# Kernel optimization log

Measured on AMD Instinct MI355X. Metric: run time of the kernel, lower is better.

Reference implementation:

```python
import jax, jax.numpy as jnp
import numpy as np

T, B, D = 1024, 512, 128
NQ = 8          # n_qubits == hidden_dim
H = NQ


def setup_inputs() -> dict:
    key = jax.random.key(0)
    ks = jax.random.split(key, 13)
    fan_in = D + H
    s = 1.0 / np.sqrt(fan_in)
    def lin(kw, kb):
        W = jax.random.uniform(kw, (NQ, fan_in), jnp.float32, -s, s)
        b = jax.random.uniform(kb, (NQ,), jnp.float32, -s, s)
        return W, b
    Wf, bf = lin(ks[0], ks[1])
    Wi, bi = lin(ks[2], ks[3])
    Wu, bu = lin(ks[4], ks[5])
    Wo, bo = lin(ks[6], ks[7])
    qwf = jax.random.normal(ks[8], (NQ,), jnp.float32)
    qwi = jax.random.normal(ks[9], (NQ,), jnp.float32)
    qwu = jax.random.normal(ks[10], (NQ,), jnp.float32)
    qwo = jax.random.normal(ks[11], (NQ,), jnp.float32)
    inputs = jax.random.normal(ks[12], (T, B, D), jnp.float32)
    return {"inputs": inputs,
            "Wf": Wf, "bf": bf, "Wi": Wi, "bi": bi,
            "Wu": Wu, "bu": bu, "Wo": Wo, "bo": bo,
            "qwf": qwf, "qwi": qwi, "qwu": qwu, "qwo": qwo}


def _qgate(z, qw):
    # Analytic form of the circuit: RX(x_i) then RY(w_i) per wire, CNOT ladder,
    # expval(Z_0). Z_0 commutes with the CNOT ladder, so only wire 0 matters:
    # <Z_0> = cos(x_0) * cos(w_0). Gate = sigmoid(<Z_0>), shape [B].
    return jax.nn.sigmoid(jnp.cos(z[:, 0]) * jnp.cos(qw[0]))


def reference(inputs, Wf, bf, Wi, bi, Wu, bu, Wo, bo, qwf, qwi, qwu, qwo):
    batch = inputs.shape[1]
    hx0 = jnp.zeros((batch, H), inputs.dtype)
    cx0 = jnp.zeros((batch, H), inputs.dtype)

    def step(carry, x):
        hx, cx = carry
        comb = jnp.concatenate([x, hx], axis=1)          # [B, D+H]
        f = _qgate(comb @ Wf.T + bf, qwf)                # [B]
        i = _qgate(comb @ Wi.T + bi, qwi)                # [B]
        g = jnp.tanh(comb @ Wu.T + bu)                   # [B, H]
        o = _qgate(comb @ Wo.T + bo, qwo)                # [B]
        cx = f[:, None] * cx + i[:, None] * g
        hx = o[:, None] * jnp.tanh(cx)
        return (hx, cx), hx

    (hx, cx), outputs = jax.lax.scan(step, (hx0, cx0), inputs)
    return outputs, hx, cx
```

## Files before the change

### kernel.cpp

```cpp
#include <hip/hip_runtime.h>
#include <cstddef>

#define TT 1024
#define BB 512
#define DD 128
#define FAN 136

__device__ __forceinline__ float v_exp2(float x){ float d; asm("v_exp_f32 %0, %1" : "=v"(d) : "v"(x)); return d; }
__device__ __forceinline__ float v_rcp (float x){ float d; asm("v_rcp_f32 %0, %1" : "=v"(d) : "v"(x)); return d; }
__device__ __forceinline__ float v_cosr(float x){ float d; asm("v_cos_f32 %0, %1" : "=v"(d) : "v"(x)); return d; }

__device__ __forceinline__ float fast_cos(float x){
    float r = x * 0.15915494309189535f;
    r = r - floorf(r);
    return v_cosr(r);
}
__device__ __forceinline__ float fast_sigmoid(float x){
    float e = v_exp2(x * -1.4426950408889634f);
    return v_rcp(1.0f + e);
}
__device__ __forceinline__ float fast_tanh(float x){
    float e = v_exp2(x * 2.8853900817779268f);
    return 1.0f - 2.0f * v_rcp(e + 1.0f);
}

__global__ __launch_bounds__(256) void qlstm_zx(
    const float* __restrict__ x,
    const float* __restrict__ Wf, const float* __restrict__ bf,
    const float* __restrict__ Wi, const float* __restrict__ bi,
    const float* __restrict__ Wu, const float* __restrict__ bu,
    const float* __restrict__ Wo, const float* __restrict__ bo,
    float* __restrict__ Z)
{
    __shared__ float xs[256 * 33];
    const int tid = threadIdx.x;
    const int t  = blockIdx.x >> 1;
    const int b0 = (blockIdx.x & 1) * 256;

    float acc[8];
    #pragma unroll
    for (int k = 0; k < 8; ++k) acc[k] = bu[k];
    float af = bf[0], ai = bi[0], ao = bo[0];

    const float* xbase = x + ((size_t)t * BB + b0) * DD;

    for (int dc = 0; dc < 4; ++dc) {
        #pragma unroll
        for (int i = 0; i < 8; ++i) {
            int idx = i * 256 + tid;
            int row = idx >> 3, cg = idx & 7;
            const float4 v = *reinterpret_cast<const float4*>(xbase + row * DD + dc * 32 + cg * 4);
            float* d = &xs[row * 33 + cg * 4];
            d[0] = v.x; d[1] = v.y; d[2] = v.z; d[3] = v.w;
        }
        __syncthreads();

        const int base = dc * 32;
        #pragma unroll
        for (int d = 0; d < 32; ++d) {
            const float xv = xs[tid * 33 + d];
            const int wc = base + d;
            #pragma unroll
            for (int k = 0; k < 8; ++k) acc[k] = fmaf(xv, Wu[k * FAN + wc], acc[k]);
            af = fmaf(xv, Wf[wc], af);
            ai = fmaf(xv, Wi[wc], ai);
            ao = fmaf(xv, Wo[wc], ao);
        }
        __syncthreads();
    }

    float* zb = Z + (size_t)t * 12 * BB + b0 + tid;
    #pragma unroll
    for (int k = 0; k < 8; ++k) zb[k * BB] = acc[k];
    zb[8 * BB] = af; zb[9 * BB] = ai; zb[10 * BB] = ao;
}

__global__ __launch_bounds__(64) void qlstm_rec(
    const float* __restrict__ Z,
    const float* __restrict__ Wf, const float* __restrict__ Wi,
    const float* __restrict__ Wu, const float* __restrict__ Wo,
    const float* __restrict__ qwf, const float* __restrict__ qwi,
    const float* __restrict__ qwo,
    float* __restrict__ out)
{
    const int l = threadIdx.x;
    const int g = l >> 3, j = l & 7;
    const int b = blockIdx.x * 8 + g;

    float wu_[8], wf_[8], wi_[8], wo_[8];
    #pragma unroll
    for (int m = 0; m < 8; ++m) {
        const int k = j ^ m;
        wu_[m] = Wu[j * FAN + 128 + k];
        wf_[m] = Wf[128 + k];
        wi_[m] = Wi[128 + k];
        wo_[m] = Wo[128 + k];
    }
    const float cqf = cosf(qwf[0]);
    const float cqi = cosf(qwi[0]);
    const float cqo = cosf(qwo[0]);

    float a[8];
    #pragma unroll
    for (int m = 0; m < 8; ++m) a[m] = 0.f;
    float c = 0.f;

    const float* z0 = Z + b;
    float zu = z0[(size_t)j * BB];
    float zf = z0[8 * BB], zi = z0[9 * BB], zo = z0[10 * BB];

    const int obase = blockIdx.x * 64 + l;

    for (int t = 0; t < TT; ++t) {
        float nzu = 0.f, nzf = 0.f, nzi = 0.f, nzo = 0.f;
        if (t + 1 < TT) {
            const float* zn = Z + (size_t)(t + 1) * 12 * BB + b;
            nzu = zn[(size_t)j * BB];
            nzf = zn[8 * BB]; nzi = zn[9 * BB]; nzo = zn[10 * BB];
        }

        float du = zu, df = zf, di = zi, dq = zo;
        #pragma unroll
        for (int m = 0; m < 8; ++m) {
            du = fmaf(a[m], wu_[m], du);
            df = fmaf(a[m], wf_[m], df);
            di = fmaf(a[m], wi_[m], di);
            dq = fmaf(a[m], wo_[m], dq);
        }

        const float f  = fast_sigmoid(fast_cos(df) * cqf);
        const float i_ = fast_sigmoid(fast_cos(di) * cqi);
        const float o_ = fast_sigmoid(fast_cos(dq) * cqo);
        const float gg = fast_tanh(du);

        c = fmaf(f, c, i_ * gg);
        const float h = o_ * fast_tanh(c);

        out[(size_t)t * 4096 + obase] = h;

        a[0] = h;
        a[1] = __shfl_xor(a[0], 1);
        a[2] = __shfl_xor(a[0], 2);
        a[3] = __shfl_xor(a[1], 2);
        a[4] = __shfl_xor(a[0], 4);
        a[5] = __shfl_xor(a[1], 4);
        a[6] = __shfl_xor(a[2], 4);
        a[7] = __shfl_xor(a[3], 4);

        zu = nzu; zf = nzf; zi = nzi; zo = nzo;
    }

    out[4194304 + obase] = a[0];
    out[4198400 + obase] = c;
}

extern "C" void kernel_launch(void* const* d_in, const int* in_sizes, int n_in,
                              void* d_out, int out_size, void* d_ws, size_t ws_size,
                              hipStream_t stream) {
    const float* x   = (const float*)d_in[0];
    const float* Wf  = (const float*)d_in[1];
    const float* bf  = (const float*)d_in[2];
    const float* Wi  = (const float*)d_in[3];
    const float* bi  = (const float*)d_in[4];
    const float* Wu  = (const float*)d_in[5];
    const float* bu  = (const float*)d_in[6];
    const float* Wo  = (const float*)d_in[7];
    const float* bo  = (const float*)d_in[8];
    const float* qwf = (const float*)d_in[9];
    const float* qwi = (const float*)d_in[10];
    const float* qwo = (const float*)d_in[12];
    float* out = (float*)d_out;
    float* Z   = (float*)d_ws;

    qlstm_zx<<<2048, 256, 0, stream>>>(x, Wf, bf, Wi, bi, Wu, bu, Wo, bo, Z);
    qlstm_rec<<<64, 64, 0, stream>>>(Z, Wf, Wi, Wu, Wo, qwf, qwi, qwo, out);
}
```

Before: 723.9 us.

## Rewrite projection and recurrence kernels with lane-split dot products, blocked Z layout, DPP exchange

The input-projection kernel now splits each batch row's 128-wide dot products across 16 lanes, keeping weights in registers and reducing partial sums with DPP and ds_swizzle, instead of staging x through shared memory. Z is stored in a batch-blocked layout so each recurrence workgroup reads a contiguous 96-float chunk per timestep. The recurrence prefetches eight timesteps ahead into registers, replaces __shfl_xor with DPP moves for the hidden-state exchange, and uses v_fract for range reduction. The aim is less latency per serial step and better projection bandwidth, at the cost of many more registers in the projection kernel and reliance on exact DPP lane patterns being correct.

Measured after the change: 594.3 us. -17.9%, faster.

```diff
diff --git a/kernel.cpp b/kernel.cpp
--- a/kernel.cpp
+++ b/kernel.cpp
@@ -3,28 +3,33 @@
 
 #define TT 1024
 #define BB 512
-#define DD 128
 #define FAN 136
 
-__device__ __forceinline__ float v_exp2(float x){ float d; asm("v_exp_f32 %0, %1" : "=v"(d) : "v"(x)); return d; }
-__device__ __forceinline__ float v_rcp (float x){ float d; asm("v_rcp_f32 %0, %1" : "=v"(d) : "v"(x)); return d; }
-__device__ __forceinline__ float v_cosr(float x){ float d; asm("v_cos_f32 %0, %1" : "=v"(d) : "v"(x)); return d; }
+__device__ __forceinline__ float v_exp2 (float x){ float d; asm("v_exp_f32 %0, %1"   : "=v"(d) : "v"(x)); return d; }
+__device__ __forceinline__ float v_rcp  (float x){ float d; asm("v_rcp_f32 %0, %1"   : "=v"(d) : "v"(x)); return d; }
+__device__ __forceinline__ float v_cosr (float x){ float d; asm("v_cos_f32 %0, %1"   : "=v"(d) : "v"(x)); return d; }
+__device__ __forceinline__ float v_fract(float x){ float d; asm("v_fract_f32 %0, %1" : "=v"(d) : "v"(x)); return d; }
 
 __device__ __forceinline__ float fast_cos(float x){
-    float r = x * 0.15915494309189535f;
-    r = r - floorf(r);
-    return v_cosr(r);
+    return v_cosr(v_fract(x * 0.15915494309189535f));
 }
 __device__ __forceinline__ float fast_sigmoid(float x){
-    float e = v_exp2(x * -1.4426950408889634f);
-    return v_rcp(1.0f + e);
+    return v_rcp(1.0f + v_exp2(x * -1.4426950408889634f));
 }
 __device__ __forceinline__ float fast_tanh(float x){
-    float e = v_exp2(x * 2.8853900817779268f);
-    return 1.0f - 2.0f * v_rcp(e + 1.0f);
-}
-
-__global__ __launch_bounds__(256) void qlstm_zx(
+    return 1.0f - 2.0f * v_rcp(v_exp2(x * 2.8853900817779268f) + 1.0f);
+}
+
+template<int CTRL>
+__device__ __forceinline__ float dppf(float x){
+    return __int_as_float(__builtin_amdgcn_mov_dpp(__float_as_int(x), CTRL, 0xF, 0xF, true));
+}
+template<int PAT>
+__device__ __forceinline__ float swzf(float x){
+    return __int_as_float(__builtin_amdgcn_ds_swizzle(__float_as_int(x), PAT));
+}
+
+__global__ __launch_bounds__(256) void qlstm_zx2(
     const float* __restrict__ x,
     const float* __restrict__ Wf, const float* __restrict__ bf,
     const float* __restrict__ Wi, const float* __restrict__ bi,
@@ -32,50 +37,82 @@
     const float* __restrict__ Wo, const float* __restrict__ bo,
     float* __restrict__ Z)
 {
-    __shared__ float xs[256 * 33];
     const int tid = threadIdx.x;
-    const int t  = blockIdx.x >> 1;
-    const int b0 = (blockIdx.x & 1) * 256;
-
-    float acc[8];
-    #pragma unroll
-    for (int k = 0; k < 8; ++k) acc[k] = bu[k];
-    float af = bf[0], ai = bi[0], ao = bo[0];
-
-    const float* xbase = x + ((size_t)t * BB + b0) * DD;
-
-    for (int dc = 0; dc < 4; ++dc) {
-        #pragma unroll
-        for (int i = 0; i < 8; ++i) {
-            int idx = i * 256 + tid;
-            int row = idx >> 3, cg = idx & 7;
-            const float4 v = *reinterpret_cast<const float4*>(xbase + row * DD + dc * 32 + cg * 4);
-            float* d = &xs[row * 33 + cg * 4];
-            d[0] = v.x; d[1] = v.y; d[2] = v.z; d[3] = v.w;
+    const int bl  = tid >> 4;
+    const int ds  = tid & 15;
+    const int t   = blockIdx.x >> 1;
+    const int b0  = (blockIdx.x & 1) * 256;
+
+    float w[11][8];
+    #pragma unroll
+    for (int k = 0; k < 8; ++k) {
+        const float4 lo = *reinterpret_cast<const float4*>(Wu + k * FAN + ds * 8);
+        const float4 hi = *reinterpret_cast<const float4*>(Wu + k * FAN + ds * 8 + 4);
+        w[k][0]=lo.x; w[k][1]=lo.y; w[k][2]=lo.z; w[k][3]=lo.w;
+        w[k][4]=hi.x; w[k][5]=hi.y; w[k][6]=hi.z; w[k][7]=hi.w;
+    }
+    {
+        const float4 lo = *reinterpret_cast<const float4*>(Wf + ds * 8);
+        const float4 hi = *reinterpret_cast<const float4*>(Wf + ds * 8 + 4);
+        w[8][0]=lo.x; w[8][1]=lo.y; w[8][2]=lo.z; w[8][3]=lo.w;
+        w[8][4]=hi.x; w[8][5]=hi.y; w[8][6]=hi.z; w[8][7]=hi.w;
+    }
+    {
+        const float4 lo = *reinterpret_cast<const float4*>(Wi + ds * 8);
+        const float4 hi = *reinterpret_cast<const float4*>(Wi + ds * 8 + 4);
+        w[9][0]=lo.x; w[9][1]=lo.y; w[9][2]=lo.z; w[9][3]=lo.w;
+        w[9][4]=hi.x; w[9][5]=hi.y; w[9][6]=hi.z; w[9][7]=hi.w;
+    }
+    {
+        const float4 lo = *reinterpret_cast<const float4*>(Wo + ds * 8);
+        const float4 hi = *reinterpret_cast<const float4*>(Wo + ds * 8 + 4);
+        w[10][0]=lo.x; w[10][1]=lo.y; w[10][2]=lo.z; w[10][3]=lo.w;
+        w[10][4]=hi.x; w[10][5]=hi.y; w[10][6]=hi.z; w[10][7]=hi.w;
+    }
+
+    float my_bias = 0.f;
+    if (ds <  8) my_bias = bu[ds];
+    if (ds ==  8) my_bias = bf[0];
+    if (ds ==  9) my_bias = bi[0];
+    if (ds == 10) my_bias = bo[0];
+
+    const float* xp = x + ((size_t)(t * BB + b0 + bl)) * 128 + ds * 8;
+
+    for (int it = 0; it < 16; ++it) {
+        const int b = b0 + it * 16 + bl;
+        const float4 xa = *reinterpret_cast<const float4*>(xp);
+        const float4 xb = *reinterpret_cast<const float4*>(xp + 4);
+        const float xr[8] = {xa.x, xa.y, xa.z, xa.w, xb.x, xb.y, xb.z, xb.w};
+
+        float acc[11];
+        #pragma unroll
+        for (int k = 0; k < 11; ++k) {
+            float s = 0.f;
+            #pragma unroll
+            for (int e = 0; e < 8; ++e) s = fmaf(xr[e], w[k][e], s);
+            acc[k] = s;
         }
-        __syncthreads();
-
-        const int base = dc * 32;
-        #pragma unroll
-        for (int d = 0; d < 32; ++d) {
-            const float xv = xs[tid * 33 + d];
-            const int wc = base + d;
-            #pragma unroll
-            for (int k = 0; k < 8; ++k) acc[k] = fmaf(xv, Wu[k * FAN + wc], acc[k]);
-            af = fmaf(xv, Wf[wc], af);
-            ai = fmaf(xv, Wi[wc], ai);
-            ao = fmaf(xv, Wo[wc], ao);
+        #pragma unroll
+        for (int k = 0; k < 11; ++k) {
+            float v = acc[k];
+            v += dppf<0xB1>(v);
+            v += dppf<0x4E>(v);
+            v += swzf<0x101F>(v);
+            v += swzf<0x201F>(v);
+            acc[k] = v;
         }
-        __syncthreads();
-    }
-
-    float* zb = Z + (size_t)t * 12 * BB + b0 + tid;
-    #pragma unroll
-    for (int k = 0; k < 8; ++k) zb[k * BB] = acc[k];
-    zb[8 * BB] = af; zb[9 * BB] = ai; zb[10 * BB] = ao;
-}
-
-__global__ __launch_bounds__(64) void qlstm_rec(
+        float val = acc[0];
+        #pragma unroll
+        for (int k = 1; k < 11; ++k) val = (ds == k) ? acc[k] : val;
+        val += my_bias;
+        if (ds < 11)
+            Z[(size_t)t * 6144 + (size_t)(b >> 3) * 96 + ds * 8 + (b & 7)] = val;
+
+        xp += 16 * 128;
+    }
+}
+
+__global__ __launch_bounds__(64) void qlstm_rec2(
     const float* __restrict__ Z,
     const float* __restrict__ Wf, const float* __restrict__ Wi,
     const float* __restrict__ Wu, const float* __restrict__ Wo,
@@ -85,7 +122,7 @@
 {
     const int l = threadIdx.x;
     const int g = l >> 3, j = l & 7;
-    const int b = blockIdx.x * 8 + g;
+    const int bid = blockIdx.x;
 
     float wu_[8], wf_[8], wi_[8], wo_[8];
     #pragma unroll
@@ -96,62 +133,71 @@
         wi_[m] = Wi[128 + k];
         wo_[m] = Wo[128 + k];
     }
-    const float cqf = cosf(qwf[0]);
-    const float cqi = cosf(qwi[0]);
-    const float cqo = cosf(qwo[0]);
+    const float cqf = fast_cos(qwf[0]);
+    const float cqi = fast_cos(qwi[0]);
+    const float cqo = fast_cos(qwo[0]);
 
     float a[8];
     #pragma unroll
     for (int m = 0; m < 8; ++m) a[m] = 0.f;
-    float c = 0.f;
-
-    const float* z0 = Z + b;
-    float zu = z0[(size_t)j * BB];
-    float zf = z0[8 * BB], zi = z0[9 * BB], zo = z0[10 * BB];
-
-    const int obase = blockIdx.x * 64 + l;
-
-    for (int t = 0; t < TT; ++t) {
-        float nzu = 0.f, nzf = 0.f, nzi = 0.f, nzo = 0.f;
-        if (t + 1 < TT) {
-            const float* zn = Z + (size_t)(t + 1) * 12 * BB + b;
-            nzu = zn[(size_t)j * BB];
-            nzf = zn[8 * BB]; nzi = zn[9 * BB]; nzo = zn[10 * BB];
+    float c = 0.f, h = 0.f;
+
+    const float* zb = Z + (size_t)bid * 96;
+    const int ou = j * 8 + g;
+    const int of = 64 + g, oi = 72 + g, oo = 80 + g;
+
+    float zr[8][4];
+    #pragma unroll
+    for (int p = 0; p < 8; ++p) {
+        const float* s = zb + (size_t)p * 6144;
+        zr[p][0] = s[ou]; zr[p][1] = s[of]; zr[p][2] = s[oi]; zr[p][3] = s[oo];
+    }
+
+    float* op = out + bid * 64 + l;
+
+    for (int t0 = 0; t0 < TT; t0 += 8) {
+        #pragma unroll
+        for (int p = 0; p < 8; ++p) {
+            const float zu = zr[p][0], zf = zr[p][1], zi = zr[p][2], zo = zr[p][3];
+            {
+                const int tn = t0 + p + 8;
+                const float* s = zb + (size_t)(tn < TT ? tn : TT - 1) * 6144;
+                zr[p][0] = s[ou]; zr[p][1] = s[of]; zr[p][2] = s[oi]; zr[p][3] = s[oo];
+            }
+
+            float du = zu, df = zf, di = zi, dq = zo;
+            #pragma unroll
+            for (int m = 0; m < 8; ++m) {
+                du = fmaf(a[m], wu_[m], du);
+                df = fmaf(a[m], wf_[m], df);
+                di = fmaf(a[m], wi_[m], di);
+                dq = fmaf(a[m], wo_[m], dq);
+            }
+
+            const float f  = fast_sigmoid(fast_cos(df) * cqf);
+            const float i_ = fast_sigmoid(fast_cos(di) * cqi);
+            const float o_ = fast_sigmoid(fast_cos(dq) * cqo);
+            const float gg = fast_tanh(du);
+
+            c = fmaf(f, c, i_ * gg);
+            h = o_ * fast_tanh(c);
+
+            *op = h; op += 4096;
+
+            a[0] = h;
+            a[1] = dppf<0xB1>(h);
+            a[2] = dppf<0x4E>(h);
+            a[3] = dppf<0x1B>(h);
+            const float h7 = dppf<0x141>(h);
+            a[7] = h7;
+            a[6] = dppf<0xB1>(h7);
+            a[5] = dppf<0x4E>(h7);
+            a[4] = dppf<0x1B>(h7);
         }
-
-        float du = zu, df = zf, di = zi, dq = zo;
-        #pragma unroll
-        for (int m = 0; m < 8; ++m) {
-            du = fmaf(a[m], wu_[m], du);
-            df = fmaf(a[m], wf_[m], df);
-            di = fmaf(a[m], wi_[m], di);
-            dq = fmaf(a[m], wo_[m], dq);
-        }
-
-        const float f  = fast_sigmoid(fast_cos(df) * cqf);
-        const float i_ = fast_sigmoid(fast_cos(di) * cqi);
-        const float o_ = fast_sigmoid(fast_cos(dq) * cqo);
-        const float gg = fast_tanh(du);
-
-        c = fmaf(f, c, i_ * gg);
-        const float h = o_ * fast_tanh(c);
-
-        out[(size_t)t * 4096 + obase] = h;
-
-        a[0] = h;
-        a[1] = __shfl_xor(a[0], 1);
-        a[2] = __shfl_xor(a[0], 2);
-        a[3] = __shfl_xor(a[1], 2);
-        a[4] = __shfl_xor(a[0], 4);
-        a[5] = __shfl_xor(a[1], 4);
-        a[6] = __shfl_xor(a[2], 4);
-        a[7] = __shfl_xor(a[3], 4);
-
-        zu = nzu; zf = nzf; zi = nzi; zo = nzo;
-    }
-
-    out[4194304 + obase] = a[0];
-    out[4198400 + obase] = c;
+    }
+
+    out[4194304 + bid * 64 + l] = h;
+    out[4198400 + bid * 64 + l] = c;
 }
 
 extern "C" void kernel_launch(void* const* d_in, const int* in_sizes, int n_in,
@@ -172,6 +218,6 @@
     float* out = (float*)d_out;
     float* Z   = (float*)d_ws;
 
-    qlstm_zx<<<2048, 256, 0, stream>>>(x, Wf, bf, Wi, bi, Wu, bu, Wo, bo, Z);
-    qlstm_rec<<<64, 64, 0, stream>>>(Z, Wf, Wi, Wu, Wo, qwf, qwi, qwo, out);
-}
+    qlstm_zx2<<<2048, 256, 0, stream>>>(x, Wf, bf, Wi, bi, Wu, bu, Wo, bo, Z);
+    qlstm_rec2<<<64, 64, 0, stream>>>(Z, Wf, Wi, Wu, Wo, qwf, qwi, qwo, out);
+}
```
